# Performance work log

Measured on AMD Instinct MI355X. Metric: run time of the kernel, lower is better.

Reference implementation:

```python
import jax, jax.numpy as jnp
import numpy as np

B, S, HID = 4, 2048, 1024
E, K, H = 8, 2, 8          # num_experts, topk, num_heads
DK = HID // H              # head_qk_dim = 128
DV = HID // H              # head_v_dim = 128
CAP = int(S * 1.0)         # capacity_len = int((S*K)/K * capacity)
CHUNK = 64
EPS = 1e-5


def setup_inputs() -> dict:
    key = jax.random.key(0)
    ks = jax.random.split(key, 12)
    std = 0.02  # ~ xavier_uniform with gain 2**-2.5
    return {
        "x": jax.random.normal(ks[0], (B, S, HID), jnp.float32),
        "gate_w": jax.random.normal(ks[1], (E, HID), jnp.float32) * std,
        "q_w": jax.random.normal(ks[2], (HID, HID), jnp.float32) * std,
        "k_w": jax.random.normal(ks[3], (E, HID, HID), jnp.float32) * std,
        "v_w": jax.random.normal(ks[4], (E, HID, HID), jnp.float32) * std,
        "fmq1_w": jax.random.normal(ks[5], (DK, DK), jnp.float32) * std,
        "fmq2_w": jax.random.normal(ks[6], (DK, DK), jnp.float32) * std,
        "fmk1_w": jax.random.normal(ks[7], (DK, DK), jnp.float32) * std,
        "fmk2_w": jax.random.normal(ks[8], (DK, DK), jnp.float32) * std,
        "norm_w": jnp.ones((DV,), jnp.float32),
        "o_w": jax.random.normal(ks[9], (HID, HID), jnp.float32) * std,
    }


def chunk_linear_attn(q, k, v):
    # q,k: (Bt, T, H, DK); v: (Bt, T, H, DV). Causal linear attention, chunked.
    Bt, T, Hh, Dk = q.shape
    Dv = v.shape[-1]
    nc = T // CHUNK
    q = q * (Dk ** -0.5)
    qc = q.reshape(Bt, nc, CHUNK, Hh, Dk).transpose(1, 0, 2, 3, 4)
    kc = k.reshape(Bt, nc, CHUNK, Hh, Dk).transpose(1, 0, 2, 3, 4)
    vc = v.reshape(Bt, nc, CHUNK, Hh, Dv).transpose(1, 0, 2, 3, 4)
    causal = jnp.tril(jnp.ones((CHUNK, CHUNK), q.dtype))
    def step(Sst, qkv):
        qb, kb, vb = qkv  # (Bt, CHUNK, H, D)
        attn = jnp.einsum('bihd,bjhd->bhij', qb, kb) * causal
        intra = jnp.einsum('bhij,bjhe->bihe', attn, vb)
        inter = jnp.einsum('bihd,bhde->bihe', qb, Sst)
        Sst = Sst + jnp.einsum('bjhd,bjhe->bhde', kb, vb)
        return Sst, intra + inter
    S0 = jnp.zeros((Bt, Hh, Dk, Dv), q.dtype)
    _, o = jax.lax.scan(step, S0, (qc, kc, vc))
    return o.transpose(1, 0, 2, 3, 4).reshape(Bt, T, Hh, Dv)


def _forward(x, gate_w, q_w, k_w, v_w, fmq1_w, fmq2_w, fmk1_w, fmk2_w, norm_w, o_w):
    b, s0, d = x.shape
    # ---- routing ----
    logits = jnp.einsum('bsd,ed->bse', x, gate_w)
    scores = jax.nn.softmax(logits.astype(jnp.float32), axis=-1)
    rw, sel = jax.lax.top_k(scores, K)                 # (b, s0, K)
    rw = (rw / rw.sum(-1, keepdims=True)).astype(x.dtype)
    routing_mask = jax.nn.one_hot(sel, E, dtype=jnp.int32).sum(2)  # (b, s0, E)
    # ---- transform: sort-by-(batch,expert), capacity gather ----
    s = s0 * K
    x_rep = jnp.repeat(x, K, axis=1).reshape(b * s, d)  # repeat_interleave over seq
    sel_flat = sel.reshape(b * s).astype(jnp.int32)
    batch_idx = jnp.repeat(jnp.arange(b, dtype=jnp.int32), s)
    combined = batch_idx * E + sel_flat
    sorted_indices = jnp.argsort(combined)              # stable in jax
    x_sorted = x_rep[sorted_indices]
    tokens = routing_mask.sum(axis=1)                   # (b, E) tokens per group
    flat_off = (jnp.cumsum(tokens, axis=1) + (jnp.arange(b, dtype=jnp.int32) * s)[:, None]).reshape(-1)
    starts = jnp.concatenate([jnp.zeros((1,), flat_off.dtype), flat_off[:-1]])
    idx = starts[:, None] + jnp.arange(CAP, dtype=flat_off.dtype)[None, :]
    shift = jnp.maximum(tokens.reshape(-1) - CAP, 0)    # keep last CAP tokens
    tidx = idx + shift[:, None]                         # (b*E, CAP)
    dmask = tidx < flat_off[:, None]
    tidx = jnp.where(dmask, tidx, 0)
    xe = x_sorted[tidx.reshape(-1)].reshape(b * E, CAP, d) * dmask[..., None].astype(x.dtype)
    xe = xe.reshape(b, E, CAP, d).transpose(1, 0, 2, 3)  # (E, b, CAP, d)
    # ---- projections + Hadamard feature maps ----
    q = jnp.einsum('ebtc,kc->ebtk', xe, q_w).reshape(E, b, CAP, H, DK)
    k = jnp.einsum('ebtc,ekc->ebtk', xe, k_w).reshape(E, b, CAP, H, DK)
    v = jnp.einsum('ebtc,ekc->ebtk', xe, v_w).reshape(E, b, CAP, H, DV)
    q = jnp.einsum('...d,kd->...k', q, fmq1_w) * jnp.einsum('...d,kd->...k', q, fmq2_w)
    k = jnp.einsum('...d,kd->...k', k, fmk1_w) * jnp.einsum('...d,kd->...k', k, fmk2_w)
    # ---- causal chunked linear attention per (expert, batch) slot ----
    o = chunk_linear_attn(q.reshape(E * b, CAP, H, DK),
                          k.reshape(E * b, CAP, H, DK),
                          v.reshape(E * b, CAP, H, DV))
    # ---- reconstruct: scatter-add back, undo sort, weighted topk combine ----
    oflat = o.reshape(E, b, CAP, H, DV).transpose(1, 0, 2, 3, 4).reshape(b * E * CAP, H, DV)
    oflat = oflat * dmask.reshape(-1)[:, None, None].astype(o.dtype)
    res = jnp.zeros((b * s, H, DV), o.dtype).at[tidx.reshape(-1)].add(oflat)
    inv = jnp.argsort(sorted_indices)
    restored = res[inv].reshape(b, s0, K, H, DV)
    out = (restored * rw[..., None, None]).sum(axis=2)   # (b, s0, H, DV)
    # RMSNorm over head_v_dim, merge heads, output proj
    out = out * jax.lax.rsqrt(jnp.mean(out * out, axis=-1, keepdims=True) + EPS) * norm_w
    out = out.reshape(b, s0, H * DV)
    return jnp.einsum('bsv,dv->bsd', out, o_w)


def reference(x, gate_w, q_w, k_w, v_w, fmq1_w, fmq2_w, fmk1_w, fmk2_w, norm_w, o_w):
    return _forward(x, gate_w, q_w, k_w, v_w, fmq1_w, fmq2_w, fmk1_w, fmk2_w, norm_w, o_w)
```

## Files before the change

### kernel.cpp

```cpp
#include <hip/hip_runtime.h>
#include <stdint.h>

typedef unsigned short u16;
typedef unsigned int   u32;
typedef __attribute__((ext_vector_type(4))) float f32x4;
typedef __attribute__((ext_vector_type(4))) u32   u32x4;
typedef __attribute__((ext_vector_type(8))) __bf16 bf16x8;

#define MFMA16(a,b,c) __builtin_amdgcn_mfma_f32_16x16x32_bf16((a),(b),(c),0,0,0)

#define QSCALE 0.08838834764831845f
#define RMAX   20480

__device__ __forceinline__ float bf2f(u16 x){ u32 u=((u32)x)<<16; float f; __builtin_memcpy(&f,&u,4); return f; }
__device__ __forceinline__ u16 f2bf(float f){ u32 u; __builtin_memcpy(&u,&f,4); u = u + 0x7FFFu + ((u>>16)&1u); return (u16)(u>>16); }
__device__ __forceinline__ u32 pack2(float a, float b){ return (u32)f2bf(a) | ((u32)f2bf(b)<<16); }

__device__ __forceinline__ void gl_lds(const u16* g, u16* l){
  __builtin_amdgcn_global_load_lds(
      (const __attribute__((address_space(1))) void*)g,
      (__attribute__((address_space(3))) void*)l, 16, 0, 0);
}

#define TSW(row, oct) ((row)*72 + ((((oct) ^ (((row)>>3)&7)))<<3))


__device__ __forceinline__ void cvt_body(const float* __restrict__ s, u16* __restrict__ d,
                                         long n8, int lb, int nb){
  long idx = (long)lb*256 + threadIdx.x;
  long stride = (long)nb*256;
  for (long i=idx; i<n8; i+=stride){
    const float* p = s + i*8;
    f32x4 a = *(const f32x4*)p;
    f32x4 b = *(const f32x4*)(p+4);
    u32x4 o;
    o[0]=pack2(a[0],a[1]); o[1]=pack2(a[2],a[3]); o[2]=pack2(b[0],b[1]); o[3]=pack2(b[2],b[3]);
    *(u32x4*)(d + i*8) = o;
  }
}

__device__ __forceinline__ void route_body(const float* __restrict__ x, const float* __restrict__ gw,
  int* __restrict__ sel, float* __restrict__ rw, u16* __restrict__ xb, int lb)
{
  int w = threadIdx.x>>6, lane = threadIdx.x&63;
  int tok = lb*4 + w;
  const float* xr = x + (size_t)tok*1024 + lane*16;
  f32x4 xv[4];
  #pragma unroll
  for (int q=0;q<4;q++) xv[q] = *(const f32x4*)(xr + q*4);
  {
    u16* xrow = xb + (size_t)tok*1024 + lane*16;
    u32x4 o0, o1;
    o0[0]=pack2(xv[0][0],xv[0][1]); o0[1]=pack2(xv[0][2],xv[0][3]);
    o0[2]=pack2(xv[1][0],xv[1][1]); o0[3]=pack2(xv[1][2],xv[1][3]);
    o1[0]=pack2(xv[2][0],xv[2][1]); o1[1]=pack2(xv[2][2],xv[2][3]);
    o1[2]=pack2(xv[3][0],xv[3][1]); o1[3]=pack2(xv[3][2],xv[3][3]);
    *(u32x4*)xrow     = o0;
    *(u32x4*)(xrow+8) = o1;
  }
  float part[8];
  #pragma unroll
  for (int e=0;e<8;e++){
    const float* g = gw + e*1024 + lane*16;
    float s = 0.f;
    #pragma unroll
    for (int q=0;q<4;q++){
      f32x4 gv = *(const f32x4*)(g + q*4);
      s += xv[q][0]*gv[0] + xv[q][1]*gv[1] + xv[q][2]*gv[2] + xv[q][3]*gv[3];
    }
    part[e]=s;
  }
  #pragma unroll
  for (int e=0;e<8;e++){
    float v = part[e];
    #pragma unroll
    for (int off=32; off>0; off>>=1) v += __shfl_xor(v, off, 64);
    part[e]=v;
  }
  if (lane==0){
    int i0=0; float m0=part[0];
    #pragma unroll
    for (int e=1;e<8;e++) if (part[e]>m0){ m0=part[e]; i0=e; }
    int i1=0; float m1=-3.4e38f;
    #pragma unroll
    for (int e=0;e<8;e++) if (e!=i0 && part[e]>m1){ m1=part[e]; i1=e; }
    sel[tok] = i0 | (i1<<8);
    float e1 = expf(m1-m0);
    float inv = 1.f/(1.f+e1);
    rw[tok*2+0] = inv;
    rw[tok*2+1] = e1*inv;
  }
}

__device__ __forceinline__ void prep_body(
  const float* __restrict__ q_w, const float* __restrict__ k_w,
  const float* __restrict__ fmq1, const float* __restrict__ fmq2,
  const float* __restrict__ fmk1, const float* __restrict__ fmk2,
  u16* __restrict__ wA, u16* __restrict__ wB, int l, u16* shmem)
{
  int gi = l>>3;
  int c0 = (l&7)*128;
  const float* fm; const float* ws; u16* wd;
  if (gi < 8)      { int h=gi;    fm=fmq1; ws=q_w + (size_t)h*131072; wd=wA + (size_t)h*262144; }
  else if (gi < 16){ int h=gi-8;  fm=fmq2; ws=q_w + (size_t)h*131072; wd=wA + (size_t)h*262144 + 131072; }
  else if (gi < 80){ int t=gi-16, e=t>>3, h=t&7; fm=fmk1; ws=k_w + (size_t)(e*8+h)*131072; wd=wB + (size_t)e*2097152 + (size_t)h*262144; }
  else             { int t=gi-80, e=t>>3, h=t&7; fm=fmk2; ws=k_w + (size_t)(e*8+h)*131072; wd=wB + (size_t)e*2097152 + (size_t)h*262144 + 131072; }
  u16* Af = shmem;
  u16* Bf = shmem + 128*136;
  int tid = threadIdx.x;
  for (int i=tid; i<4096; i+=256){
    int row = i>>5, col = (i&31)*4;
    f32x4 v = *(const f32x4*)&fm[row*128 + col];
    u16* dp = &Af[row*136 + col];
    *(u32*)dp     = pack2(v[0],v[1]);
    *(u32*)(dp+2) = pack2(v[2],v[3]);
  }
  for (int i=tid; i<4096; i+=256){
    int dd = i>>5, cq = (i&31)*4;
    f32x4 v = *(const f32x4*)&ws[(size_t)dd*1024 + c0 + cq];
    #pragma unroll
    for (int j=0;j<4;j++){
      int c = cq+j;
      Bf[c*136 + (dd ^ (((c>>2)&3)<<3))] = f2bf(v[j]);
    }
  }
  __syncthreads();
  int lane=tid&63, w=tid>>6, wr=w>>1, wc=w&1, lc=lane&15, lr=lane>>4;
  const f32x4 Z4 = {0.f,0.f,0.f,0.f};
  f32x4 acc[4][4];
  #pragma unroll
  for (int i=0;i<4;i++){
    #pragma unroll
    for (int j=0;j<4;j++) acc[i][j]=Z4;
  }
  #pragma unroll
  for (int kk=0; kk<4; ++kk){
    bf16x8 a[4], b[4];
    #pragma unroll
    for (int mi=0;mi<4;mi++)
      a[mi] = *(const bf16x8*)&Af[(wr*64+mi*16+lc)*136 + kk*32 + lr*8];
    #pragma unroll
    for (int ni=0;ni<4;ni++){
      int c = wc*64+ni*16+lc;
      b[ni] = *(const bf16x8*)&Bf[c*136 + ((kk*32 + lr*8) ^ (((c>>2)&3)<<3))];
    }
    #pragma unroll
    for (int mi=0;mi<4;mi++){
      #pragma unroll
      for (int ni=0;ni<4;ni++)
        acc[mi][ni] = MFMA16(a[mi], b[ni], acc[mi][ni]);
    }
  }
  int r0=lr*4;
  #pragma unroll
  for (int mi=0;mi<4;mi++){
    #pragma unroll
    for (int ni=0;ni<4;ni++){
      int col = c0 + wc*64 + ni*16 + lc;
      #pragma unroll
      for (int r=0;r<4;r++){
        int row = wr*64 + mi*16 + r0 + r;
        wd[(size_t)row*1024 + col] = f2bf(acc[mi][ni][r]);
      }
    }
  }
}

__global__ __launch_bounds__(256) void k_pre(
  const float* __restrict__ x, const float* __restrict__ gw,
  int* __restrict__ sel, float* __restrict__ rw,
  const float* __restrict__ q_w, const float* __restrict__ k_w,
  const float* __restrict__ fmq1, const float* __restrict__ fmq2,
  const float* __restrict__ fmk1, const float* __restrict__ fmk2,
  u16* __restrict__ wA, u16* __restrict__ wB, u16* __restrict__ xb,
  const float* __restrict__ v_w, u16* __restrict__ wVb,
  const float* __restrict__ o_w, u16* __restrict__ wOb, int* __restrict__ done)
{
  __shared__ __align__(16) u16 shmem[2*128*136];
  int bid = blockIdx.x;
  if (bid==0 && threadIdx.x==0) *done = 0;
  if (bid < 2048)      route_body(x, gw, sel, rw, xb, bid);
  else if (bid < 3200) prep_body(q_w, k_w, fmq1, fmq2, fmk1, fmk2, wA, wB, bid-2048, shmem);
  else if (bid < 3456) cvt_body(v_w, wVb, 1048576L, bid-3200, 256);
  else                 cvt_body(o_w, wOb, 131072L, bid-3456, 32);
}

__global__ __launch_bounds__(256) void k_count(const int* __restrict__ sel,
  int* __restrict__ slot_of, int* __restrict__ src_of, int* __restrict__ meta,
  int* __restrict__ done)
{
  int g = blockIdx.x, b = g>>3, e = g&7;
  int tid = threadIdx.x;
  __shared__ int cn[256];
  unsigned char ex[16];
  int cnt=0;
  #pragma unroll
  for (int i=0;i<16;i++){
    int t = tid*16+i;
    int sv = sel[b*2048 + (t>>1)];
    int ee = (t&1) ? ((sv>>8)&255) : (sv&255);
    ex[i]=(unsigned char)ee;
    cnt += (ee==e);
  }
  cn[tid]=cnt;
  __syncthreads();
  for (int off=1; off<256; off<<=1){
    int v = (tid>=off) ? cn[tid-off] : 0;
    __syncthreads();
    cn[tid] += v;
    __syncthreads();
  }
  int total = cn[255];
  int run = cn[tid]-cnt;
  int shift = total>2048 ? total-2048 : 0;
  #pragma unroll
  for (int i=0;i<16;i++){
    int t = tid*16+i;
    if (ex[i]==e){
      int j = run - shift;
      run++;
      slot_of[b*4096 + t] = (j>=0)? j : -1;
      if (j>=0) src_of[g*2048 + j] = t;
    }
  }
  if (tid==0){
    meta[g]=total;
    __threadfence();
    if (atomicAdd(done,1)==31){
      int basev=0, t=0;
      meta[96]=0;
      for (int gg=0; gg<32; ++gg){
        int n = atomicAdd(&meta[gg],0);
        int nact = n<2048 ? n : 2048;
        int npad = (nact+127)&~127;
        meta[32+gg]=nact;
        meta[64+gg]=npad;
        meta[129+gg]=(nact+63)>>6;
        for (int i=0;i<(npad>>7);++i) meta[192+t++]=gg;
        basev += npad;
        meta[97+gg]=basev;
      }
      meta[161]=basev;
    }
  }
}

__global__ __launch_bounds__(256) void k_gather(const u16* __restrict__ xb,
  const int* __restrict__ src_of, const int* __restrict__ meta, u16* __restrict__ xg,
  int* __restrict__ tokmap)
{
  int g = blockIdx.y, jb = blockIdx.x;
  int npad = meta[64+g];
  if (jb*64 >= npad) return;
  int nact = meta[32+g], base = meta[96+g];
  int tid = threadIdx.x;
  int j = jb*64 + (tid>>2);
  int quart = tid&3;
  int src = (j<nact) ? src_of[g*2048+j] : -1;
  int token = (src>=0) ? ((g>>3)*2048 + (src>>1)) : 0;
  if (quart==0) tokmap[base+j] = token;
  u16* orow = xg + ((size_t)(base+j))*1024 + quart*256;
  if (src>=0){
    const u16* xr = xb + (size_t)token*1024 + quart*256;
    #pragma unroll
    for (int i=0;i<256;i+=8) *(u32x4*)(orow+i) = *(const u32x4*)(xr+i);
  } else {
    u32x4 z = {0,0,0,0};
    #pragma unroll
    for (int i=0;i<256;i+=8) *(u32x4*)(orow+i)=z;
  }
}

__global__ __launch_bounds__(512) void k_gemmQKV(const u16* __restrict__ xb, const u16* __restrict__ xg,
  const u16* __restrict__ wA, const u16* __restrict__ wB, const u16* __restrict__ wVb,
  u16* __restrict__ qh, u16* __restrict__ kh, u16* __restrict__ vv, const int* __restrict__ meta)
{
  int bid = blockIdx.x;
  int role, tm, tn;
  const u16 *A, *Wp; u16* outB;
  if (bid < 512){
    role=0; int l=bid, xcd=l&7, jj=l>>3, jd=jj>>3;
    tm=xcd*8+jd; tn=jj&7;
    A=xb; Wp=wA + (size_t)tn*262144; outB=qh;
  } else if (bid < 1792){
    role=1; int l=bid-512, xcd=l&7, jj=l>>3, jd=jj>>3;
    tm=xcd*20+jd; tn=jj&7;
    if (tm*128 >= meta[161]) return;
    A=xg; Wp=wB + (size_t)(meta[192+tm]&7)*2097152 + (size_t)tn*262144; outB=kh;
  } else {
    role=2; int l=bid-1792, xcd=l&7, jj=l>>3, jd=jj>>2;
    tm=xcd*20+jd; tn=jj&3;
    if (tm*128 >= meta[161]) return;
    A=xg; Wp=wVb + (size_t)(meta[192+tm]&7)*1048576 + (size_t)tn*262144; outB=vv;
  }

  __shared__ __align__(16) u16 smem[73728];

  int tid=threadIdx.x, lane=tid&63;
  int w=tid>>6, wr=w>>2, wc=w&3, lc=lane&15, lr=lane>>4;
  int swz = lc&7;
  const f32x4 Z4 = {0.f,0.f,0.f,0.f};
  f32x4 acc[4][4];
  #pragma unroll
  for(int i=0;i<4;i++){
    #pragma unroll
    for(int j2=0;j2<4;j2++) acc[i][j2]=Z4;
  }
  size_t lanoff = (size_t)(tid>>3)*1024 + (size_t)(((tid&7)^((tid>>3)&7))*8);
  const u16* Ag = A  + (size_t)tm*131072 + lanoff;
  const u16* Bg = Wp + lanoff;
  int lo = tid*8;

  #define STAGEF(ao, bo, kt) { \
    const u16* ga = Ag + (kt)*64; const u16* gb = Bg + (kt)*64; \
    gl_lds(ga,                 &smem[(ao) + lo]); \
    gl_lds(ga + (size_t)65536, &smem[(ao) + 4096 + lo]); \
    gl_lds(gb,                  &smem[(bo) + lo]); \
    gl_lds(gb + (size_t)65536,  &smem[(bo) + 4096 + lo]); \
    gl_lds(gb + (size_t)131072, &smem[(bo) + 8192 + lo]); \
    gl_lds(gb + (size_t)196608, &smem[(bo) + 12288 + lo]); }

  STAGEF(0, 24576, 0);
  STAGEF(8192, 40960, 1);
  int cur = 0;
  for (int kt=0; kt<16; ++kt){
    if (kt<15) asm volatile("s_waitcnt vmcnt(6)" ::: "memory");
    else       asm volatile("s_waitcnt vmcnt(0)" ::: "memory");
    __builtin_amdgcn_s_barrier();
    if (kt<14){
      int nid = kt+2; nid -= (nid/3)*3;
      STAGEF(nid*8192, 24576+nid*16384, kt+2);
    }
    int ao = cur*8192, bo = 24576 + cur*16384;
    __builtin_amdgcn_s_setprio(1);
    #pragma unroll
    for (int kk=0; kk<2; ++kk){
      bf16x8 a[4], b[4];
      #pragma unroll
      for (int mi=0;mi<4;mi++){
        int row = wr*64+mi*16+lc;
        a[mi] = *(const bf16x8*)&smem[ao + row*64 + (((kk*4+lr)^swz)<<3)];
      }
      #pragma unroll
      for (int ni=0;ni<4;ni++){
        int row = wc*64+ni*16+lc;
        b[ni] = *(const bf16x8*)&smem[bo + row*64 + (((kk*4+lr)^swz)<<3)];
      }
      #pragma unroll
      for (int mi=0;mi<4;mi++){
        #pragma unroll
        for (int ni=0;ni<4;ni++)
          acc[mi][ni] = MFMA16(a[mi], b[ni], acc[mi][ni]);
      }
    }
    __builtin_amdgcn_s_setprio(0);
    cur = (cur==2)?0:cur+1;
  }
  __syncthreads();
  if (role < 2){
    if (wc >= 2){
      #pragma unroll
      for (int mi=0;mi<4;mi++){
        #pragma unroll
        for (int ni=0;ni<4;ni++){
          int col = (wc-2)*64 + ni*16 + lc;
          #pragma unroll
          for (int r=0;r<4;r++)
            ((float*)smem)[(wr*64+mi*16+lr*4+r)*129 + col] = acc[mi][ni][r];
        }
      }
    }
    __syncthreads();
    if (wc < 2){
      float scl = (role==0) ? QSCALE : 1.0f;
      #pragma unroll
      for (int mi=0;mi<4;mi++){
        #pragma unroll
        for (int ni=0;ni<4;ni++){
          int col = wc*64 + ni*16 + lc;
          #pragma unroll
          for (int r=0;r<4;r++){
            int row = wr*64+mi*16+lr*4+r;
            float v = acc[mi][ni][r] * ((float*)smem)[row*129 + col] * scl;
            outB[(size_t)(tm*128+row)*1024 + tn*128 + col] = f2bf(v);
          }
        }
      }
    }
  } else {
    #pragma unroll
    for (int mi=0;mi<4;mi++){
      #pragma unroll
      for (int ni=0;ni<4;ni++){
        int col = tn*256 + wc*64 + ni*16 + lc;
        #pragma unroll
        for (int r=0;r<4;r++){
          int row = tm*128 + wr*64 + mi*16 + lr*4 + r;
          outB[(size_t)row*1024 + col] = f2bf(acc[mi][ni][r]);
        }
      }
    }
  }
  #undef STAGEF
}

__global__ __launch_bounds__(512) void k_gemmO(const u16* __restrict__ A, const u16* __restrict__ W,
  float* __restrict__ outF)
{
  int tnN = gridDim.x;
  int bid = blockIdx.y*tnN + blockIdx.x;
  int chunk = gridDim.y >> 3;
  int xcd = bid & 7, j = bid >> 3;
  int jd = j / tnN;
  int tm = xcd*chunk + jd;
  int tn = j - jd*tnN;

  __shared__ __align__(16) u16 smem[73728];

  int tid=threadIdx.x, lane=tid&63;
  int w=tid>>6, wr=w>>2, wc=w&3, lc=lane&15, lr=lane>>4;
  int swz = lc&7;
  const f32x4 Z4 = {0.f,0.f,0.f,0.f};
  f32x4 acc[4][4];
  #pragma unroll
  for(int i=0;i<4;i++){
    #pragma unroll
    for(int j2=0;j2<4;j2++) acc[i][j2]=Z4;
  }
  size_t lanoff = (size_t)(tid>>3)*1024 + (size_t)(((tid&7)^((tid>>3)&7))*8);
  const u16* Ag = A + (size_t)tm*131072 + lanoff;
  const u16* Bg = W + (size_t)tn*262144 + lanoff;
  int lo = tid*8;

  #define STAGEO(ao, bo, kt) { \
    const u16* ga = Ag + (kt)*64; const u16* gb = Bg + (kt)*64; \
    gl_lds(ga,                 &smem[(ao) + lo]); \
    gl_lds(ga + (size_t)65536, &smem[(ao) + 4096 + lo]); \
    gl_lds(gb,                  &smem[(bo) + lo]); \
    gl_lds(gb + (size_t)65536,  &smem[(bo) + 4096 + lo]); \
    gl_lds(gb + (size_t)131072, &smem[(bo) + 8192 + lo]); \
    gl_lds(gb + (size_t)196608, &smem[(bo) + 12288 + lo]); }

  STAGEO(0, 24576, 0);
  STAGEO(8192, 40960, 1);
  int cur = 0;
  for (int kt=0; kt<16; ++kt){
    if (kt<15) asm volatile("s_waitcnt vmcnt(6)" ::: "memory");
    else       asm volatile("s_waitcnt vmcnt(0)" ::: "memory");
    __builtin_amdgcn_s_barrier();
    if (kt<14){
      int nid = kt+2; nid -= (nid/3)*3;
      STAGEO(nid*8192, 24576+nid*16384, kt+2);
    }
    int ao = cur*8192, bo = 24576 + cur*16384;
    __builtin_amdgcn_s_setprio(1);
    #pragma unroll
    for (int kk=0; kk<2; ++kk){
      bf16x8 a[4], b[4];
      #pragma unroll
      for (int mi=0;mi<4;mi++){
        int row = wr*64+mi*16+lc;
        a[mi] = *(const bf16x8*)&smem[ao + row*64 + (((kk*4+lr)^swz)<<3)];
      }
      #pragma unroll
      for (int ni=0;ni<4;ni++){
        int row = wc*64+ni*16+lc;
        b[ni] = *(const bf16x8*)&smem[bo + row*64 + (((kk*4+lr)^swz)<<3)];
      }
      #pragma unroll
      for (int mi=0;mi<4;mi++){
        #pragma unroll
        for (int ni=0;ni<4;ni++)
          acc[mi][ni] = MFMA16(a[mi], b[ni], acc[mi][ni]);
      }
    }
    __builtin_amdgcn_s_setprio(0);
    cur = (cur==2)?0:cur+1;
  }
  #pragma unroll
  for (int mi=0;mi<4;mi++){
    #pragma unroll
    for (int ni=0;ni<4;ni++){
      int col = tn*256 + wc*64 + ni*16 + lc;
      #pragma unroll
      for (int r=0;r<4;r++){
        int row = tm*128 + wr*64 + mi*16 + lr*4 + r;
        outF[(size_t)row*1024 + col] = acc[mi][ni][r];
      }
    }
  }
  #undef STAGEO
}

__global__ __launch_bounds__(256,1) void k_attn(const u16* __restrict__ qv, const u16* __restrict__ kv,
  const u16* __restrict__ vv, u16* __restrict__ o, const int* __restrict__ meta,
  const int* __restrict__ tokmap)
{
  int g = blockIdx.x>>3, h = blockIdx.x&7;
  int nch = meta[129+g];
  if (nch==0) return;
  int base = meta[96+g];
  __shared__ __align__(16) u16 Qs[64*136];
  __shared__ __align__(16) u16 Ks[64*136];
  __shared__ __align__(16) u16 KTs[128*72];
  __shared__ __align__(16) u16 VTs[128*72];
  __shared__ __align__(16) u16 Ts[2*128*136];
  __shared__ __align__(16) u16 Ps[64*72];
  int tid=threadIdx.x, w=tid>>6, lane=tid&63;
  int wr=w>>1, wc=w&1;
  int lr=lane>>4, lc=lane&15;
  {
    u32x4 z={0,0,0,0};
    for (int i=tid; i<128*136/8; i+=256) *(u32x4*)&Ts[i*8]=z;
  }
  const f32x4 Z4 = {0.f,0.f,0.f,0.f};
  f32x4 accT[4][4];
  #pragma unroll
  for (int i=0;i<4;i++){
    #pragma unroll
    for (int j=0;j<4;j++) accT[i][j]=Z4;
  }
  __syncthreads();
  const u16* kb = kv + (size_t)base*1024 + h*128;
  const u16* vb = vv + (size_t)base*1024 + h*128;
  u16* ob = o + (size_t)base*1024 + h*128;
  int tso = 0;

  for (int c=0; c<nch; ++c){
    #pragma unroll
    for (int it=0; it<4; ++it){
      int id = tid + it*256;
      int row = id>>4, kc = id&15;
      int tok = tokmap[base + c*64 + row];
      *(u32x4*)&Qs[row*136 + kc*8] = *(const u32x4*)(qv + (size_t)tok*1024 + h*128 + kc*8);
      *(u32x4*)&Ks[row*136 + kc*8] = *(const u32x4*)(kb + (size_t)(c*64+row)*1024 + kc*8);
    }
    #pragma unroll
    for (int it=0; it<4; ++it){
      int id = tid + it*256;
      int j = id>>4, dg = id&15;
      int col = (((j>>3) ^ (dg&7))<<3) + (j&7);
      u32x4 kx = *(const u32x4*)(kb + (size_t)(c*64+j)*1024 + dg*8);
      u32x4 vx = *(const u32x4*)(vb + (size_t)(c*64+j)*1024 + dg*8);
      #pragma unroll
      for (int t=0;t<4;t++){
        KTs[(dg*8+t*2  )*72 + col] = (u16)(kx[t]&0xffff);
        KTs[(dg*8+t*2+1)*72 + col] = (u16)(kx[t]>>16);
        VTs[(dg*8+t*2  )*72 + col] = (u16)(vx[t]&0xffff);
        VTs[(dg*8+t*2+1)*72 + col] = (u16)(vx[t]>>16);
      }
    }
    __syncthreads();
    bf16x8 qf[2][4];
    #pragma unroll
    for (int ti=0; ti<2; ++ti){
      #pragma unroll
      for (int ks=0; ks<4; ++ks)
        qf[ti][ks] = *(const bf16x8*)&Qs[(wr*32+ti*16+lc)*136 + ks*32 + lr*8];
    }
    f32x4 accO[2][4];
    #pragma unroll
    for (int i=0;i<2;i++){
      #pragma unroll
      for (int j=0;j<4;j++) accO[i][j]=Z4;
    }
    #pragma unroll
    for (int ks=0; ks<4; ++ks){
      bf16x8 bt[4];
      #pragma unroll
      for (int te=0; te<4; ++te)
        bt[te] = *(const bf16x8*)&Ts[tso + (wc*64+te*16+lc)*136 + ks*32 + lr*8];
      #pragma unroll
      for (int ti=0; ti<2; ++ti){
        #pragma unroll
        for (int te=0; te<4; ++te)
          accO[ti][te] = MFMA16(qf[ti][ks], bt[te], accO[ti][te]);
      }
    }
    f32x4 accP[2][2];
    #pragma unroll
    for (int i=0;i<2;i++){
      #pragma unroll
      for (int j=0;j<2;j++) accP[i][j]=Z4;
    }
    #pragma unroll
    for (int ks=0; ks<4; ++ks){
      bf16x8 bk[2];
      #pragma unroll
      for (int tj=0; tj<2; ++tj)
        bk[tj] = *(const bf16x8*)&Ks[(wc*32+tj*16+lc)*136 + ks*32 + lr*8];
      #pragma unroll
      for (int ti=0; ti<2; ++ti){
        #pragma unroll
        for (int tj=0; tj<2; ++tj)
          accP[ti][tj] = MFMA16(qf[ti][ks], bk[tj], accP[ti][tj]);
      }
    }
    #pragma unroll
    for (int ti=0; ti<2; ++ti){
      #pragma unroll
      for (int tj=0; tj<2; ++tj){
        #pragma unroll
// ... 91 lines not shown
      u32x4 v = *(const u32x4*)(orow + q*8);
      #pragma unroll
      for (int t=0;t<4;t++){
        acc[q*8+t*2]   += wgt * bf2f((u16)(v[t]&0xffff));
        acc[q*8+t*2+1] += wgt * bf2f((u16)(v[t]>>16));
      }
    }
  }
  float ssq=0.f;
  #pragma unroll
  for (int i=0;i<16;i++) ssq += acc[i]*acc[i];
  ssq += __shfl_xor(ssq,1,64);
  ssq += __shfl_xor(ssq,2,64);
  ssq += __shfl_xor(ssq,4,64);
  float sc = rsqrtf(ssq*(1.f/128.f) + 1e-5f);
  int cbase = (lane&7)*16;
  u32x4 o0, o1;
  #pragma unroll
  for (int t=0;t<4;t++)
    o0[t] = pack2(acc[2*t]*sc*nw[cbase+2*t], acc[2*t+1]*sc*nw[cbase+2*t+1]);
  #pragma unroll
  for (int t=0;t<4;t++)
    o1[t] = pack2(acc[8+2*t]*sc*nw[cbase+8+2*t], acc[8+2*t+1]*sc*nw[cbase+8+2*t+1]);
  u16* fp = fin + (size_t)tok*1024 + lane*16;
  *(u32x4*)fp     = o0;
  *(u32x4*)(fp+8) = o1;
}

extern "C" void kernel_launch(void* const* d_in, const int* in_sizes, int n_in,
                              void* d_out, int out_size, void* d_ws, size_t ws_size,
                              hipStream_t stream)
{
  (void)in_sizes; (void)n_in;
  const float* x     = (const float*)d_in[0];
  const float* gate  = (const float*)d_in[1];
  const float* q_w   = (const float*)d_in[2];
  const float* k_w   = (const float*)d_in[3];
  const float* v_w   = (const float*)d_in[4];
  const float* fmq1  = (const float*)d_in[5];
  const float* fmq2  = (const float*)d_in[6];
  const float* fmk1  = (const float*)d_in[7];
  const float* fmk2  = (const float*)d_in[8];
  const float* norm_w= (const float*)d_in[9];
  const float* o_w   = (const float*)d_in[10];
  float* out = (float*)d_out;

  uint8_t* ws = (uint8_t*)d_ws;
  size_t off = 0;
  auto alloc = [&](size_t bytes)->void*{ void* p = ws + off; off += (bytes + 255) & ~(size_t)255; return p; };
  int*   meta = (int*)alloc(4096);
  int*   sel  = (int*)alloc(8192*4);
  float* rwb  = (float*)alloc(8192*2*4);
  int*   slot = (int*)alloc(16384*4);
  int*   srcf = (int*)alloc((size_t)32*2048*4);
  int*   tokm = (int*)alloc((size_t)RMAX*4);
  int*   done = (int*)alloc(256);
  u16* wA  = (u16*)alloc((size_t)2097152*2);
  u16* wB  = (u16*)alloc((size_t)8*2097152*2);
  u16* wOb = (u16*)alloc((size_t)1048576*2);
  u16* xb  = (u16*)alloc((size_t)8192*1024*2);
  u16* xg  = (u16*)alloc((size_t)RMAX*1024*2);
  u16* qh  = (u16*)alloc((size_t)8192*1024*2);
  u16* kh  = (u16*)alloc((size_t)RMAX*1024*2);
  u16* vv  = (u16*)alloc((size_t)RMAX*1024*2);
  if (off > ws_size){
    hipMemsetAsync(d_out, 0x7F, (size_t)out_size*4, stream);
    return;
  }
  u16* wVb = (u16*)d_out;
  u16* ob  = xg;
  u16* fin = qh;

  k_pre<<<3488,256,0,stream>>>(x, gate, sel, rwb, q_w, k_w, fmq1, fmq2, fmk1, fmk2, wA, wB, xb, v_w, wVb, o_w, wOb, done);
  k_count<<<32,256,0,stream>>>(sel, slot, srcf, meta, done);
  k_gather<<<dim3(32,32),256,0,stream>>>(xb, srcf, meta, xg, tokm);
  k_gemmQKV<<<2432,512,0,stream>>>(xb, xg, wA, wB, wVb, qh, kh, vv, meta);
  k_attn<<<256,256,0,stream>>>(qh, kh, vv, ob, meta, tokm);
  k_comb<<<2048,256,0,stream>>>(ob, sel, rwb, slot, meta, norm_w, fin);
  k_gemmO<<<dim3(4,64),512,0,stream>>>(fin, wOb, out);
}
```

Before: 411.5 us.

## Enlarge QKV GEMM M-tile to 256 rows with double-buffered interleaved staging

Each workgroup of the fused Q/K/V GEMM now computes a 256-row tile instead of 128, so each warp holds 8x4 accumulators and reuses loaded B fragments across twice as many rows. Per-group row padding moves to multiples of 256, and RMAX grows to fit the extra padding. The old three-stage pipeline becomes a two-buffer scheme where the next A and B slices are issued in pieces between MFMA groups, with a launch bound requesting two workgroups per CU. The aim is fewer weight reloads and fewer workgroups. The cost is more wasted padded rows per expert group, more accumulator registers, and workspace buffers swapped so the K weights now live in the output buffer.

```diff
diff --git a/kernel.cpp b/kernel.cpp
--- a/kernel.cpp
+++ b/kernel.cpp
@@ -10,7 +10,7 @@
 #define MFMA16(a,b,c) __builtin_amdgcn_mfma_f32_16x16x32_bf16((a),(b),(c),0,0,0)
 
 #define QSCALE 0.08838834764831845f
-#define RMAX   20480
+#define RMAX   24576
 
 __device__ __forceinline__ float bf2f(u16 x){ u32 u=((u32)x)<<16; float f; __builtin_memcpy(&f,&u,4); return f; }
 __device__ __forceinline__ u16 f2bf(float f){ u32 u; __builtin_memcpy(&u,&f,4); u = u + 0x7FFFu + ((u>>16)&1u); return (u16)(u>>16); }
@@ -232,11 +232,11 @@
       for (int gg=0; gg<32; ++gg){
         int n = atomicAdd(&meta[gg],0);
         int nact = n<2048 ? n : 2048;
-        int npad = (nact+127)&~127;
+        int npad = (nact+255)&~255;
         meta[32+gg]=nact;
         meta[64+gg]=npad;
         meta[129+gg]=(nact+63)>>6;
-        for (int i=0;i<(npad>>7);++i) meta[192+t++]=gg;
+        for (int i=0;i<(npad>>8);++i) meta[192+t++]=gg;
         basev += npad;
         meta[97+gg]=basev;
       }
@@ -271,102 +271,113 @@
   }
 }
 
-__global__ __launch_bounds__(512) void k_gemmQKV(const u16* __restrict__ xb, const u16* __restrict__ xg,
+__global__ __launch_bounds__(512,2) void k_gemmQKV(const u16* __restrict__ xb, const u16* __restrict__ xg,
   const u16* __restrict__ wA, const u16* __restrict__ wB, const u16* __restrict__ wVb,
   u16* __restrict__ qh, u16* __restrict__ kh, u16* __restrict__ vv, const int* __restrict__ meta)
 {
   int bid = blockIdx.x;
   int role, tm, tn;
   const u16 *A, *Wp; u16* outB;
-  if (bid < 512){
+  if (bid < 256){
     role=0; int l=bid, xcd=l&7, jj=l>>3, jd=jj>>3;
-    tm=xcd*8+jd; tn=jj&7;
+    tm=xcd*4+jd; tn=jj&7;
     A=xb; Wp=wA + (size_t)tn*262144; outB=qh;
-  } else if (bid < 1792){
-    role=1; int l=bid-512, xcd=l&7, jj=l>>3, jd=jj>>3;
-    tm=xcd*20+jd; tn=jj&7;
-    if (tm*128 >= meta[161]) return;
+  } else if (bid < 1024){
+    role=1; int l=bid-256, xcd=l&7, jj=l>>3, jd=jj>>3;
+    tm=xcd*12+jd; tn=jj&7;
+    if (tm*256 >= meta[161]) return;
     A=xg; Wp=wB + (size_t)(meta[192+tm]&7)*2097152 + (size_t)tn*262144; outB=kh;
   } else {
-    role=2; int l=bid-1792, xcd=l&7, jj=l>>3, jd=jj>>2;
-    tm=xcd*20+jd; tn=jj&3;
-    if (tm*128 >= meta[161]) return;
+    role=2; int l=bid-1024, xcd=l&7, jj=l>>3, jd=jj>>2;
+    tm=xcd*12+jd; tn=jj&3;
+    if (tm*256 >= meta[161]) return;
     A=xg; Wp=wVb + (size_t)(meta[192+tm]&7)*1048576 + (size_t)tn*262144; outB=vv;
   }
 
-  __shared__ __align__(16) u16 smem[73728];
+  __shared__ __align__(16) u16 smem[65536];
 
   int tid=threadIdx.x, lane=tid&63;
   int w=tid>>6, wr=w>>2, wc=w&3, lc=lane&15, lr=lane>>4;
   int swz = lc&7;
+  int ck0 = ((lr)^swz)<<3;
+  int ck1 = ((4+lr)^swz)<<3;
+  int arow = (wr*128 + lc)*64;
+  int brow = 16384 + (wc*64 + lc)*64;
   const f32x4 Z4 = {0.f,0.f,0.f,0.f};
-  f32x4 acc[4][4];
-  #pragma unroll
-  for(int i=0;i<4;i++){
+  f32x4 acc[8][4];
+  #pragma unroll
+  for(int i=0;i<8;i++){
     #pragma unroll
     for(int j2=0;j2<4;j2++) acc[i][j2]=Z4;
   }
-  size_t lanoff = (size_t)(tid>>3)*1024 + (size_t)(((tid&7)^((tid>>3)&7))*8);
-  const u16* Ag = A  + (size_t)tm*131072 + lanoff;
-  const u16* Bg = Wp + lanoff;
-  int lo = tid*8;
-
-  #define STAGEF(ao, bo, kt) { \
-    const u16* ga = Ag + (kt)*64; const u16* gb = Bg + (kt)*64; \
-    gl_lds(ga,                 &smem[(ao) + lo]); \
-    gl_lds(ga + (size_t)65536, &smem[(ao) + 4096 + lo]); \
-    gl_lds(gb,                  &smem[(bo) + lo]); \
-    gl_lds(gb + (size_t)65536,  &smem[(bo) + 4096 + lo]); \
-    gl_lds(gb + (size_t)131072, &smem[(bo) + 8192 + lo]); \
-    gl_lds(gb + (size_t)196608, &smem[(bo) + 12288 + lo]); }
-
-  STAGEF(0, 24576, 0);
-  STAGEF(8192, 40960, 1);
-  int cur = 0;
-  for (int kt=0; kt<16; ++kt){
-    if (kt<15) asm volatile("s_waitcnt vmcnt(6)" ::: "memory");
-    else       asm volatile("s_waitcnt vmcnt(0)" ::: "memory");
-    __builtin_amdgcn_s_barrier();
-    if (kt<14){
-      int nid = kt+2; nid -= (nid/3)*3;
-      STAGEF(nid*8192, 24576+nid*16384, kt+2);
-    }
-    int ao = cur*8192, bo = 24576 + cur*16384;
-    __builtin_amdgcn_s_setprio(1);
-    #pragma unroll
-    for (int kk=0; kk<2; ++kk){
-      bf16x8 a[4], b[4];
-      #pragma unroll
-      for (int mi=0;mi<4;mi++){
-        int row = wr*64+mi*16+lc;
-        a[mi] = *(const bf16x8*)&smem[ao + row*64 + (((kk*4+lr)^swz)<<3)];
-      }
+  int rowlane = tid>>3;
+  int gch = ((tid&7)^(rowlane&7))*8;
+  const u16* Asrc = A  + (size_t)tm*262144 + (size_t)rowlane*1024 + gch;
+  const u16* Bsrc = Wp + (size_t)rowlane*1024 + gch;
+
+  #define STG2(dst, src) { \
+    gl_lds((src),         &smem[(dst) + tid*8]); \
+    gl_lds((src) + 65536, &smem[(dst) + 4096 + tid*8]); }
+
+  STG2(16384, Bsrc);
+  STG2(24576, Bsrc + 131072);
+  STG2(0,     Asrc);
+  STG2(8192,  Asrc + 131072);
+  STG2(49152, Bsrc + 64);
+  STG2(57344, Bsrc + 131072 + 64);
+
+  for (int t=0; t<16; ++t){
+    int d = (t&1)<<15;
+    bf16x8 b0[4], b1[4];
+    #pragma unroll
+    for (int j=0; j<4; ++j){
+      if (j==0){
+        if (t<15) asm volatile("s_waitcnt vmcnt(4)" ::: "memory");
+        else      asm volatile("s_waitcnt vmcnt(0)" ::: "memory");
+      }
+      __builtin_amdgcn_s_barrier();
+      if (j==0){
+        #pragma unroll
+        for (int ni=0;ni<4;ni++){
+          b0[ni] = *(const bf16x8*)&smem[d + brow + ni*1024 + ck0];
+          b1[ni] = *(const bf16x8*)&smem[d + brow + ni*1024 + ck1];
+        }
+      }
+      bf16x8 a00 = *(const bf16x8*)&smem[d + arow + (2*j  )*1024 + ck0];
+      bf16x8 a01 = *(const bf16x8*)&smem[d + arow + (2*j+1)*1024 + ck0];
+      bf16x8 a10 = *(const bf16x8*)&smem[d + arow + (2*j  )*1024 + ck1];
+      bf16x8 a11 = *(const bf16x8*)&smem[d + arow + (2*j+1)*1024 + ck1];
+      if (j==0 && t<15) STG2(((t+1)&1)<<15,            Asrc + (size_t)(t+1)*64);
+      if (j==1 && t<15) STG2((((t+1)&1)<<15) + 8192,   Asrc + 131072 + (size_t)(t+1)*64);
+      if (j==2 && t<14) STG2(d + 16384,                Bsrc + (size_t)(t+2)*64);
+      if (j==3 && t<14) STG2(d + 24576,                Bsrc + 131072 + (size_t)(t+2)*64);
+      __builtin_amdgcn_s_setprio(1);
       #pragma unroll
       for (int ni=0;ni<4;ni++){
-        int row = wc*64+ni*16+lc;
-        b[ni] = *(const bf16x8*)&smem[bo + row*64 + (((kk*4+lr)^swz)<<3)];
-      }
-      #pragma unroll
-      for (int mi=0;mi<4;mi++){
-        #pragma unroll
-        for (int ni=0;ni<4;ni++)
-          acc[mi][ni] = MFMA16(a[mi], b[ni], acc[mi][ni]);
-      }
-    }
-    __builtin_amdgcn_s_setprio(0);
-    cur = (cur==2)?0:cur+1;
-  }
+        acc[2*j  ][ni] = MFMA16(a00, b0[ni], acc[2*j  ][ni]);
+        acc[2*j+1][ni] = MFMA16(a01, b0[ni], acc[2*j+1][ni]);
+      }
+      #pragma unroll
+      for (int ni=0;ni<4;ni++){
+        acc[2*j  ][ni] = MFMA16(a10, b1[ni], acc[2*j  ][ni]);
+        acc[2*j+1][ni] = MFMA16(a11, b1[ni], acc[2*j+1][ni]);
+      }
+      __builtin_amdgcn_s_setprio(0);
+    }
+  }
+  #undef STG2
+
   __syncthreads();
   if (role < 2){
     if (wc >= 2){
       #pragma unroll
-      for (int mi=0;mi<4;mi++){
+      for (int mi=0;mi<8;mi++){
         #pragma unroll
         for (int ni=0;ni<4;ni++){
           int col = (wc-2)*64 + ni*16 + lc;
           #pragma unroll
           for (int r=0;r<4;r++)
-            ((float*)smem)[(wr*64+mi*16+lr*4+r)*129 + col] = acc[mi][ni][r];
+            ((float*)smem)[(wr*128+mi*16+lr*4+r)*128 + col] = acc[mi][ni][r];
         }
       }
     }
@@ -374,34 +385,33 @@
     if (wc < 2){
       float scl = (role==0) ? QSCALE : 1.0f;
       #pragma unroll
-      for (int mi=0;mi<4;mi++){
+      for (int mi=0;mi<8;mi++){
         #pragma unroll
         for (int ni=0;ni<4;ni++){
           int col = wc*64 + ni*16 + lc;
           #pragma unroll
           for (int r=0;r<4;r++){
-            int row = wr*64+mi*16+lr*4+r;
-            float v = acc[mi][ni][r] * ((float*)smem)[row*129 + col] * scl;
-            outB[(size_t)(tm*128+row)*1024 + tn*128 + col] = f2bf(v);
+            int row = wr*128+mi*16+lr*4+r;
+            float v = acc[mi][ni][r] * ((float*)smem)[row*128 + col] * scl;
+            outB[(size_t)(tm*256+row)*1024 + tn*128 + col] = f2bf(v);
           }
         }
       }
     }
   } else {
     #pragma unroll
-    for (int mi=0;mi<4;mi++){
+    for (int mi=0;mi<8;mi++){
       #pragma unroll
       for (int ni=0;ni<4;ni++){
         int col = tn*256 + wc*64 + ni*16 + lc;
         #pragma unroll
         for (int r=0;r<4;r++){
-          int row = tm*128 + wr*64 + mi*16 + lr*4 + r;
+          int row = tm*256 + wr*128 + mi*16 + lr*4 + r;
           outB[(size_t)row*1024 + col] = f2bf(acc[mi][ni][r]);
         }
       }
     }
   }
-  #undef STAGEF
 }
 
 __global__ __launch_bounds__(512) void k_gemmO(const u16* __restrict__ A, const u16* __restrict__ W,
@@ -749,7 +759,7 @@
   int*   tokm = (int*)alloc((size_t)RMAX*4);
   int*   done = (int*)alloc(256);
   u16* wA  = (u16*)alloc((size_t)2097152*2);
-  u16* wB  = (u16*)alloc((size_t)8*2097152*2);
+  u16* wVb = (u16*)alloc((size_t)8388608*2);
   u16* wOb = (u16*)alloc((size_t)1048576*2);
   u16* xb  = (u16*)alloc((size_t)8192*1024*2);
   u16* xg  = (u16*)alloc((size_t)RMAX*1024*2);
@@ -760,14 +770,14 @@
     hipMemsetAsync(d_out, 0x7F, (size_t)out_size*4, stream);
     return;
   }
-  u16* wVb = (u16*)d_out;
+  u16* wB  = (u16*)d_out;
   u16* ob  = xg;
   u16* fin = qh;
 
   k_pre<<<3488,256,0,stream>>>(x, gate, sel, rwb, q_w, k_w, fmq1, fmq2, fmk1, fmk2, wA, wB, xb, v_w, wVb, o_w, wOb, done);
   k_count<<<32,256,0,stream>>>(sel, slot, srcf, meta, done);
   k_gather<<<dim3(32,32),256,0,stream>>>(xb, srcf, meta, xg, tokm);
-  k_gemmQKV<<<2432,512,0,stream>>>(xb, xg, wA, wB, wVb, qh, kh, vv, meta);
+  k_gemmQKV<<<1408,512,0,stream>>>(xb, xg, wA, wB, wVb, qh, kh, vv, meta);
   k_attn<<<256,256,0,stream>>>(qh, kh, vv, ob, meta, tokm);
   k_comb<<<2048,256,0,stream>>>(ob, sel, rwb, slot, meta, norm_w, fin);
   k_gemmO<<<dim3(4,64),512,0,stream>>>(fin, wOb, out);
```

Result: no change. 405.9 us (-1.4%).

## Fuse token gather into QKV GEMM loads and share weight tiles across feature-map passes

Applied to the files above, without the earlier changes.

Removes the separate gather kernel that copied routed token rows into a packed buffer. The QKV GEMM now loads A rows directly from the bf16 input through a per-row token map, with padding rows pointing at an appended zero row. The prep kernel now computes both feature-map products from one staged weight tile, halving its block count and the reloads of q_w/k_w. Attention loads Q/K/V in a single merged loop, and buffers are reshuffled so wB lives in the output buffer. The cost is indirect, less contiguous A loads inside the GEMM.

```diff
diff --git a/kernel.cpp b/kernel.cpp
--- a/kernel.cpp
+++ b/kernel.cpp
@@ -98,24 +98,23 @@
   const float* __restrict__ fmk1, const float* __restrict__ fmk2,
   u16* __restrict__ wA, u16* __restrict__ wB, int l, u16* shmem)
 {
-  int gi = l>>3;
-  int c0 = (l&7)*128;
-  const float* fm; const float* ws; u16* wd;
-  if (gi < 8)      { int h=gi;    fm=fmq1; ws=q_w + (size_t)h*131072; wd=wA + (size_t)h*262144; }
-  else if (gi < 16){ int h=gi-8;  fm=fmq2; ws=q_w + (size_t)h*131072; wd=wA + (size_t)h*262144 + 131072; }
-  else if (gi < 80){ int t=gi-16, e=t>>3, h=t&7; fm=fmk1; ws=k_w + (size_t)(e*8+h)*131072; wd=wB + (size_t)e*2097152 + (size_t)h*262144; }
-  else             { int t=gi-80, e=t>>3, h=t&7; fm=fmk2; ws=k_w + (size_t)(e*8+h)*131072; wd=wB + (size_t)e*2097152 + (size_t)h*262144 + 131072; }
+  const float *fm1, *fm2, *ws; u16 *wd1;
+  int c0;
+  if (l < 64){
+    int h = l>>3; c0 = (l&7)*128;
+    fm1=fmq1; fm2=fmq2; ws=q_w + (size_t)h*131072;
+    wd1=wA + (size_t)h*262144;
+  } else {
+    int l2=l-64, eh=l2>>3; c0=(l2&7)*128;
+    int e=eh>>3, h=eh&7;
+    fm1=fmk1; fm2=fmk2; ws=k_w + (size_t)eh*131072;
+    wd1=wB + (size_t)e*2097152 + (size_t)h*262144;
+  }
+  u16* wd2 = wd1 + 131072;
   u16* Af = shmem;
   u16* Bf = shmem + 128*136;
   int tid = threadIdx.x;
   for (int i=tid; i<4096; i+=256){
-    int row = i>>5, col = (i&31)*4;
-    f32x4 v = *(const f32x4*)&fm[row*128 + col];
-    u16* dp = &Af[row*136 + col];
-    *(u32*)dp     = pack2(v[0],v[1]);
-    *(u32*)(dp+2) = pack2(v[2],v[3]);
-  }
-  for (int i=tid; i<4096; i+=256){
     int dd = i>>5, cq = (i&31)*4;
     f32x4 v = *(const f32x4*)&ws[(size_t)dd*1024 + c0 + cq];
     #pragma unroll
@@ -124,45 +123,58 @@
       Bf[c*136 + (dd ^ (((c>>2)&3)<<3))] = f2bf(v[j]);
     }
   }
-  __syncthreads();
   int lane=tid&63, w=tid>>6, wr=w>>1, wc=w&1, lc=lane&15, lr=lane>>4;
   const f32x4 Z4 = {0.f,0.f,0.f,0.f};
-  f32x4 acc[4][4];
-  #pragma unroll
-  for (int i=0;i<4;i++){
-    #pragma unroll
-    for (int j=0;j<4;j++) acc[i][j]=Z4;
-  }
-  #pragma unroll
-  for (int kk=0; kk<4; ++kk){
-    bf16x8 a[4], b[4];
-    #pragma unroll
-    for (int mi=0;mi<4;mi++)
-      a[mi] = *(const bf16x8*)&Af[(wr*64+mi*16+lc)*136 + kk*32 + lr*8];
-    #pragma unroll
-    for (int ni=0;ni<4;ni++){
-      int c = wc*64+ni*16+lc;
-      b[ni] = *(const bf16x8*)&Bf[c*136 + ((kk*32 + lr*8) ^ (((c>>2)&3)<<3))];
-    }
+  #pragma unroll
+  for (int pass=0; pass<2; ++pass){
+    const float* fm = pass ? fm2 : fm1;
+    u16* wd = pass ? wd2 : wd1;
+    for (int i=tid; i<4096; i+=256){
+      int row = i>>5, col = (i&31)*4;
+      f32x4 v = *(const f32x4*)&fm[row*128 + col];
+      u16* dp = &Af[row*136 + col];
+      *(u32*)dp     = pack2(v[0],v[1]);
+      *(u32*)(dp+2) = pack2(v[2],v[3]);
+    }
+    __syncthreads();
+    f32x4 acc[4][4];
+    #pragma unroll
+    for (int i=0;i<4;i++){
+      #pragma unroll
+      for (int j=0;j<4;j++) acc[i][j]=Z4;
+    }
+    #pragma unroll
+    for (int kk=0; kk<4; ++kk){
+      bf16x8 a[4], b[4];
+      #pragma unroll
+      for (int mi=0;mi<4;mi++)
+        a[mi] = *(const bf16x8*)&Af[(wr*64+mi*16+lc)*136 + kk*32 + lr*8];
+      #pragma unroll
+      for (int ni=0;ni<4;ni++){
+        int c = wc*64+ni*16+lc;
+        b[ni] = *(const bf16x8*)&Bf[c*136 + ((kk*32 + lr*8) ^ (((c>>2)&3)<<3))];
+      }
+      #pragma unroll
+      for (int mi=0;mi<4;mi++){
+        #pragma unroll
+        for (int ni=0;ni<4;ni++)
+          acc[mi][ni] = MFMA16(a[mi], b[ni], acc[mi][ni]);
+      }
+    }
+    int r0=lr*4;
     #pragma unroll
     for (int mi=0;mi<4;mi++){
       #pragma unroll
-      for (int ni=0;ni<4;ni++)
-        acc[mi][ni] = MFMA16(a[mi], b[ni], acc[mi][ni]);
-    }
-  }
-  int r0=lr*4;
-  #pragma unroll
-  for (int mi=0;mi<4;mi++){
-    #pragma unroll
-    for (int ni=0;ni<4;ni++){
-      int col = c0 + wc*64 + ni*16 + lc;
-      #pragma unroll
-      for (int r=0;r<4;r++){
-        int row = wr*64 + mi*16 + r0 + r;
-        wd[(size_t)row*1024 + col] = f2bf(acc[mi][ni][r]);
-      }
-    }
+      for (int ni=0;ni<4;ni++){
+        int col = c0 + wc*64 + ni*16 + lc;
+        #pragma unroll
+        for (int r=0;r<4;r++){
+          int row = wr*64 + mi*16 + r0 + r;
+          wd[(size_t)row*1024 + col] = f2bf(acc[mi][ni][r]);
+        }
+      }
+    }
+    __syncthreads();
   }
 }
 
@@ -180,13 +192,19 @@
   int bid = blockIdx.x;
   if (bid==0 && threadIdx.x==0) *done = 0;
   if (bid < 2048)      route_body(x, gw, sel, rw, xb, bid);
-  else if (bid < 3200) prep_body(q_w, k_w, fmq1, fmq2, fmk1, fmk2, wA, wB, bid-2048, shmem);
-  else if (bid < 3456) cvt_body(v_w, wVb, 1048576L, bid-3200, 256);
-  else                 cvt_body(o_w, wOb, 131072L, bid-3456, 32);
+  else if (bid < 2624) prep_body(q_w, k_w, fmq1, fmq2, fmk1, fmk2, wA, wB, bid-2048, shmem);
+  else if (bid < 2880) cvt_body(v_w, wVb, 1048576L, bid-2624, 256);
+  else if (bid < 2912) cvt_body(o_w, wOb, 131072L, bid-2880, 32);
+  else {
+    if (threadIdx.x < 128){
+      u32x4 z = {0,0,0,0};
+      *(u32x4*)&xb[(size_t)8192*1024 + threadIdx.x*8] = z;
+    }
+  }
 }
 
 __global__ __launch_bounds__(256) void k_count(const int* __restrict__ sel,
-  int* __restrict__ slot_of, int* __restrict__ src_of, int* __restrict__ meta,
+  int* __restrict__ slot_of, int* __restrict__ tokmap2, int* __restrict__ meta,
   int* __restrict__ done)
 {
   int g = blockIdx.x, b = g>>3, e = g&7;
@@ -220,7 +238,7 @@
       int j = run - shift;
       run++;
       slot_of[b*4096 + t] = (j>=0)? j : -1;
-      if (j>=0) src_of[g*2048 + j] = t;
+      if (j>=0) tokmap2[g*2048 + j] = b*2048 + (t>>1);
     }
   }
   if (tid==0){
@@ -245,53 +263,28 @@
   }
 }
 
-__global__ __launch_bounds__(256) void k_gather(const u16* __restrict__ xb,
-  const int* __restrict__ src_of, const int* __restrict__ meta, u16* __restrict__ xg,
-  int* __restrict__ tokmap)
-{
-  int g = blockIdx.y, jb = blockIdx.x;
-  int npad = meta[64+g];
-  if (jb*64 >= npad) return;
-  int nact = meta[32+g], base = meta[96+g];
-  int tid = threadIdx.x;
-  int j = jb*64 + (tid>>2);
-  int quart = tid&3;
-  int src = (j<nact) ? src_of[g*2048+j] : -1;
-  int token = (src>=0) ? ((g>>3)*2048 + (src>>1)) : 0;
-  if (quart==0) tokmap[base+j] = token;
-  u16* orow = xg + ((size_t)(base+j))*1024 + quart*256;
-  if (src>=0){
-    const u16* xr = xb + (size_t)token*1024 + quart*256;
-    #pragma unroll
-    for (int i=0;i<256;i+=8) *(u32x4*)(orow+i) = *(const u32x4*)(xr+i);
-  } else {
-    u32x4 z = {0,0,0,0};
-    #pragma unroll
-    for (int i=0;i<256;i+=8) *(u32x4*)(orow+i)=z;
-  }
-}
-
-__global__ __launch_bounds__(512) void k_gemmQKV(const u16* __restrict__ xb, const u16* __restrict__ xg,
+__global__ __launch_bounds__(512) void k_gemmQKV(const u16* __restrict__ xb,
   const u16* __restrict__ wA, const u16* __restrict__ wB, const u16* __restrict__ wVb,
-  u16* __restrict__ qh, u16* __restrict__ kh, u16* __restrict__ vv, const int* __restrict__ meta)
+  u16* __restrict__ qh, u16* __restrict__ kh, u16* __restrict__ vv,
+  const int* __restrict__ meta, const int* __restrict__ tokmap2)
 {
   int bid = blockIdx.x;
   int role, tm, tn;
-  const u16 *A, *Wp; u16* outB;
+  const u16 *Wp; u16* outB;
   if (bid < 512){
     role=0; int l=bid, xcd=l&7, jj=l>>3, jd=jj>>3;
     tm=xcd*8+jd; tn=jj&7;
-    A=xb; Wp=wA + (size_t)tn*262144; outB=qh;
+    Wp=wA + (size_t)tn*262144; outB=qh;
   } else if (bid < 1792){
     role=1; int l=bid-512, xcd=l&7, jj=l>>3, jd=jj>>3;
     tm=xcd*20+jd; tn=jj&7;
     if (tm*128 >= meta[161]) return;
-    A=xg; Wp=wB + (size_t)(meta[192+tm]&7)*2097152 + (size_t)tn*262144; outB=kh;
+    Wp=wB + (size_t)(meta[192+tm]&7)*2097152 + (size_t)tn*262144; outB=kh;
   } else {
     role=2; int l=bid-1792, xcd=l&7, jj=l>>3, jd=jj>>2;
     tm=xcd*20+jd; tn=jj&3;
     if (tm*128 >= meta[161]) return;
-    A=xg; Wp=wVb + (size_t)(meta[192+tm]&7)*1048576 + (size_t)tn*262144; outB=vv;
+    Wp=wVb + (size_t)(meta[192+tm]&7)*1048576 + (size_t)tn*262144; outB=vv;
   }
 
   __shared__ __align__(16) u16 smem[73728];
@@ -306,19 +299,34 @@
     #pragma unroll
     for(int j2=0;j2<4;j2++) acc[i][j2]=Z4;
   }
-  size_t lanoff = (size_t)(tid>>3)*1024 + (size_t)(((tid&7)^((tid>>3)&7))*8);
-  const u16* Ag = A  + (size_t)tm*131072 + lanoff;
-  const u16* Bg = Wp + lanoff;
+  int rowlane = tid>>3;
+  int gch = ((tid&7)^(rowlane&7))*8;
+  int tk0, tk1;
+  {
+    int r0 = tm*128 + rowlane;
+    if (role==0){
+      tk0=r0; tk1=r0+64;
+    } else {
+      int g = meta[192+tm], base = meta[96+g], nact = meta[32+g];
+      int gb = g*2048;
+      int j0 = r0 - base;
+      tk0 = (j0    < nact) ? tokmap2[gb + j0]    : 8192;
+      tk1 = (j0+64 < nact) ? tokmap2[gb + j0+64] : 8192;
+    }
+  }
+  const u16* Ap0 = xb + (size_t)tk0*1024 + gch;
+  const u16* Ap1 = xb + (size_t)tk1*1024 + gch;
+  const u16* Bg  = Wp + (size_t)rowlane*1024 + gch;
   int lo = tid*8;
 
   #define STAGEF(ao, bo, kt) { \
-    const u16* ga = Ag + (kt)*64; const u16* gb = Bg + (kt)*64; \
-    gl_lds(ga,                 &smem[(ao) + lo]); \
-    gl_lds(ga + (size_t)65536, &smem[(ao) + 4096 + lo]); \
-    gl_lds(gb,                  &smem[(bo) + lo]); \
-    gl_lds(gb + (size_t)65536,  &smem[(bo) + 4096 + lo]); \
-    gl_lds(gb + (size_t)131072, &smem[(bo) + 8192 + lo]); \
-    gl_lds(gb + (size_t)196608, &smem[(bo) + 12288 + lo]); }
+    const u16* gb_ = Bg + (kt)*64; \
+    gl_lds(Ap0 + (size_t)(kt)*64, &smem[(ao) + lo]); \
+    gl_lds(Ap1 + (size_t)(kt)*64, &smem[(ao) + 4096 + lo]); \
+    gl_lds(gb_,                  &smem[(bo) + lo]); \
+    gl_lds(gb_ + (size_t)65536,  &smem[(bo) + 4096 + lo]); \
+    gl_lds(gb_ + (size_t)131072, &smem[(bo) + 8192 + lo]); \
+    gl_lds(gb_ + (size_t)196608, &smem[(bo) + 12288 + lo]); }
 
   STAGEF(0, 24576, 0);
   STAGEF(8192, 40960, 1);
@@ -356,6 +364,8 @@
     __builtin_amdgcn_s_setprio(0);
     cur = (cur==2)?0:cur+1;
   }
+  #undef STAGEF
+
   __syncthreads();
   if (role < 2){
     if (wc >= 2){
@@ -401,7 +411,6 @@
       }
     }
   }
-  #undef STAGEF
 }
 
 __global__ __launch_bounds__(512) void k_gemmO(const u16* __restrict__ A, const u16* __restrict__ W,
@@ -494,12 +503,12 @@
 
 __global__ __launch_bounds__(256,1) void k_attn(const u16* __restrict__ qv, const u16* __restrict__ kv,
   const u16* __restrict__ vv, u16* __restrict__ o, const int* __restrict__ meta,
-  const int* __restrict__ tokmap)
+  const int* __restrict__ tokmap2)
 {
   int g = blockIdx.x>>3, h = blockIdx.x&7;
   int nch = meta[129+g];
   if (nch==0) return;
-  int base = meta[96+g];
+  int base = meta[96+g], nact = meta[32+g];
   __shared__ __align__(16) u16 Qs[64*136];
   __shared__ __align__(16) u16 Ks[64*136];
   __shared__ __align__(16) u16 KTs[128*72];
@@ -531,23 +540,20 @@
     for (int it=0; it<4; ++it){
       int id = tid + it*256;
       int row = id>>4, kc = id&15;
-      int tok = tokmap[base + c*64 + row];
-      *(u32x4*)&Qs[row*136 + kc*8] = *(const u32x4*)(qv + (size_t)tok*1024 + h*128 + kc*8);
-      *(u32x4*)&Ks[row*136 + kc*8] = *(const u32x4*)(kb + (size_t)(c*64+row)*1024 + kc*8);
-    }
-    #pragma unroll
-    for (int it=0; it<4; ++it){
-      int id = tid + it*256;
-      int j = id>>4, dg = id&15;
-      int col = (((j>>3) ^ (dg&7))<<3) + (j&7);
-      u32x4 kx = *(const u32x4*)(kb + (size_t)(c*64+j)*1024 + dg*8);
-      u32x4 vx = *(const u32x4*)(vb + (size_t)(c*64+j)*1024 + dg*8);
+      int jj = c*64 + row;
+      int tok = tokmap2[g*2048 + (jj<nact ? jj : 0)];
+      u32x4 qx = *(const u32x4*)(qv + (size_t)tok*1024 + h*128 + kc*8);
+      u32x4 kx = *(const u32x4*)(kb + (size_t)jj*1024 + kc*8);
+      u32x4 vx = *(const u32x4*)(vb + (size_t)jj*1024 + kc*8);
+      *(u32x4*)&Qs[row*136 + kc*8] = qx;
+      *(u32x4*)&Ks[row*136 + kc*8] = kx;
+      int col = (((row>>3) ^ (kc&7))<<3) + (row&7);
       #pragma unroll
       for (int t=0;t<4;t++){
-        KTs[(dg*8+t*2  )*72 + col] = (u16)(kx[t]&0xffff);
-        KTs[(dg*8+t*2+1)*72 + col] = (u16)(kx[t]>>16);
-        VTs[(dg*8+t*2  )*72 + col] = (u16)(vx[t]&0xffff);
-        VTs[(dg*8+t*2+1)*72 + col] = (u16)(vx[t]>>16);
+        KTs[(kc*8+t*2  )*72 + col] = (u16)(kx[t]&0xffff);
+        KTs[(kc*8+t*2+1)*72 + col] = (u16)(kx[t]>>16);
+        VTs[(kc*8+t*2  )*72 + col] = (u16)(vx[t]&0xffff);
+        VTs[(kc*8+t*2+1)*72 + col] = (u16)(vx[t]>>16);
       }
     }
     __syncthreads();
@@ -745,14 +751,13 @@
   int*   sel  = (int*)alloc(8192*4);
   float* rwb  = (float*)alloc(8192*2*4);
   int*   slot = (int*)alloc(16384*4);
-  int*   srcf = (int*)alloc((size_t)32*2048*4);
-  int*   tokm = (int*)alloc((size_t)RMAX*4);
+  int*   tokm2= (int*)alloc((size_t)65536*4);
   int*   done = (int*)alloc(256);
   u16* wA  = (u16*)alloc((size_t)2097152*2);
-  u16* wB  = (u16*)alloc((size_t)8*2097152*2);
+  u16* wVb = (u16*)alloc((size_t)8388608*2);
   u16* wOb = (u16*)alloc((size_t)1048576*2);
-  u16* xb  = (u16*)alloc((size_t)8192*1024*2);
-  u16* xg  = (u16*)alloc((size_t)RMAX*1024*2);
+  u16* xb  = (u16*)alloc((size_t)8193*1024*2);
+  u16* ob  = (u16*)alloc((size_t)RMAX*1024*2);
   u16* qh  = (u16*)alloc((size_t)8192*1024*2);
   u16* kh  = (u16*)alloc((size_t)RMAX*1024*2);
   u16* vv  = (u16*)alloc((size_t)RMAX*1024*2);
@@ -760,15 +765,13 @@
     hipMemsetAsync(d_out, 0x7F, (size_t)out_size*4, stream);
     return;
   }
-  u16* wVb = (u16*)d_out;
-  u16* ob  = xg;
+  u16* wB  = (u16*)d_out;
   u16* fin = qh;
 
-  k_pre<<<3488,256,0,stream>>>(x, gate, sel, rwb, q_w, k_w, fmq1, fmq2, fmk1, fmk2, wA, wB, xb, v_w, wVb, o_w, wOb, done);
-  k_count<<<32,256,0,stream>>>(sel, slot, srcf, meta, done);
-  k_gather<<<dim3(32,32),256,0,stream>>>(xb, srcf, meta, xg, tokm);
-  k_gemmQKV<<<2432,512,0,stream>>>(xb, xg, wA, wB, wVb, qh, kh, vv, meta);
-  k_attn<<<256,256,0,stream>>>(qh, kh, vv, ob, meta, tokm);
+  k_pre<<<2913,256,0,stream>>>(x, gate, sel, rwb, q_w, k_w, fmq1, fmq2, fmk1, fmk2, wA, wB, xb, v_w, wVb, o_w, wOb, done);
+  k_count<<<32,256,0,stream>>>(sel, slot, tokm2, meta, done);
+  k_gemmQKV<<<2432,512,0,stream>>>(xb, wA, wB, wVb, qh, kh, vv, meta, tokm2);
+  k_attn<<<256,256,0,stream>>>(qh, kh, vv, ob, meta, tokm2);
   k_comb<<<2048,256,0,stream>>>(ob, sel, rwb, slot, meta, norm_w, fin);
   k_gemmO<<<dim3(4,64),512,0,stream>>>(fin, wOb, out);
 }
```

New measurement: 358.5 us (median of 2 runs). 12.9% less time.
